# Performance work log

Hardware: AMD Instinct MI355X
Metric: run time of the kernel (lower is better)

The kernel has to match this reference:

```python
import jax, jax.numpy as jnp
import numpy as np

B, S, D, H = 4, 2048, 1024, 16
DH = D // H


def setup_inputs() -> dict:
    key = jax.random.key(0)
    ks = jax.random.split(key, 5)
    std = 1.0 / np.sqrt(D)
    return {
        "x": jax.random.normal(ks[0], (B, S, D), dtype=jnp.float32),
        "mask": jnp.ones((S, S), dtype=bool),  # unused by the original forward
        "Wq": jax.random.normal(ks[1], (D, D), dtype=jnp.float32) * std,
        "Wk": jax.random.normal(ks[2], (D, D), dtype=jnp.float32) * std,
        "Wv": jax.random.normal(ks[3], (D, D), dtype=jnp.float32) * std,
        "Wout": jax.random.normal(ks[4], (D, D), dtype=jnp.float32) * std,
    }


def reference(x, mask, Wq, Wk, Wv, Wout):
    n, s, d = x.shape
    scale = 1.0 / np.sqrt(DH).astype(np.float32)
    q = (x @ Wq).reshape(n, s, H, DH)
    k = (x @ Wk).reshape(n, s, H, DH)
    v = (x @ Wv).reshape(n, s, H, DH)
    # scores [n, q, k, h]; softmax over k axis (dim=-2 in original)
    attn = jnp.einsum('nqhd,nkhd->nqkh', q, k) * scale
    attn = jax.nn.softmax(attn, axis=-2)
    z = jnp.einsum('nqkh,nkhd->nqhd', attn, v).reshape(n, s, d)
    z = jnp.einsum('nqd,de->nqe', z, Wout)
    return x + z
```

## Files before the change

kernel.cpp:

```cpp
#include <hip/hip_runtime.h>

#define Bn 4
#define Sn 2048
#define Dn 1024
#define Hn 16
#define DHn 64

typedef float f32x4 __attribute__((ext_vector_type(4)));
typedef short bf16x8 __attribute__((ext_vector_type(8)));
typedef unsigned short u16;
typedef unsigned int u32;
typedef unsigned short u16x8 __attribute__((ext_vector_type(8)));
typedef unsigned short u16x4 __attribute__((ext_vector_type(4)));
typedef u32 u32x4 __attribute__((ext_vector_type(4)));

union B8 { u32x4 u; bf16x8 s; };

__device__ __forceinline__ u16 f2bf(float f){
  union { float f; u32 u; } v; v.f = f;
  return (u16)((v.u + 0x7fffu + ((v.u >> 16) & 1u)) >> 16);
}

__device__ __forceinline__ u32 pack_bf2(float lo, float hi){
  union { float f; u32 u; } a, b;
  a.f = lo; b.f = hi;
  return __builtin_amdgcn_perm(b.u + 0x8000u, a.u + 0x8000u, 0x07060302u);
}

#if __has_builtin(__builtin_amdgcn_exp2f)
#define EXP2(x) __builtin_amdgcn_exp2f(x)
#define QSCALE 0.18033688011112042f
#else
#define EXP2(x) __expf(x)
#define QSCALE 0.125f
#endif

#if __has_builtin(__builtin_amdgcn_global_load_lds)
#define G2L16(l, g) __builtin_amdgcn_global_load_lds((const __attribute__((address_space(1))) u32*)(g), \
                                                     (__attribute__((address_space(3))) u32*)(l), 16, 0, 0)
#else
#define G2L16(l, g) (*(bf16x8*)(l) = *(const bf16x8*)(g))
#endif

__global__ void cast_x_kernel(const float* __restrict__ x, u16* __restrict__ xb){
  size_t i = ((size_t)blockIdx.x * 256 + threadIdx.x) * 8;
  float4 f0 = *(const float4*)(x + i);
  float4 f1 = *(const float4*)(x + i + 4);
  u16x8 o;
  o[0]=f2bf(f0.x); o[1]=f2bf(f0.y); o[2]=f2bf(f0.z); o[3]=f2bf(f0.w);
  o[4]=f2bf(f1.x); o[5]=f2bf(f1.y); o[6]=f2bf(f1.z); o[7]=f2bf(f1.w);
  *(u16x8*)(xb + i) = o;
}

__global__ void cast_w_kernel(const float* __restrict__ w, u16* __restrict__ wt, float scale){
  __shared__ u16 tile[64*66];
  const int t = threadIdx.x;
  const int k0 = blockIdx.x * 64, n0 = blockIdx.y * 64;
  #pragma unroll
  for (int i = 0; i < 4; i++){
    int idx = i*256 + t;
    int r = idx >> 4, c4 = (idx & 15) * 4;
    float4 f = *(const float4*)(w + (size_t)(k0 + r)*Dn + n0 + c4);
    tile[r*66 + c4 + 0] = f2bf(f.x * scale);
    tile[r*66 + c4 + 1] = f2bf(f.y * scale);
    tile[r*66 + c4 + 2] = f2bf(f.z * scale);
    tile[r*66 + c4 + 3] = f2bf(f.w * scale);
  }
  __syncthreads();
  #pragma unroll
  for (int i = 0; i < 4; i++){
    int idx = i*256 + t;
    int nr = idx >> 4, kc4 = (idx & 15) * 4;
    u16x4 o;
    o[0] = tile[(kc4+0)*66 + nr];
    o[1] = tile[(kc4+1)*66 + nr];
    o[2] = tile[(kc4+2)*66 + nr];
    o[3] = tile[(kc4+3)*66 + nr];
    *(u16x4*)(wt + (size_t)(n0 + nr)*Dn + k0 + kc4) = o;
  }
}

__launch_bounds__(256)
__global__ void gemm_qkv_kernel(const u16* __restrict__ xb, const u16* __restrict__ wt_all,
                                u16* __restrict__ qb, u16* __restrict__ kb, u16* __restrict__ vb){
  __shared__ u16 As[128*32];
  __shared__ u16 Bs[128*32];
  const int t = threadIdx.x;
  const int wave = t >> 6, lane = t & 63;
  const int ln = lane & 15, quad = lane >> 4;
  const int wm = wave >> 1, wn = wave & 1;
  const int n0 = blockIdx.x * 128;
  const int m0 = blockIdx.y * 128;
  const int z  = blockIdx.z;
  const u16* wt = wt_all + (size_t)z * Dn * Dn;

  f32x4 acc[4][4] = {};

  for (int kt = 0; kt < Dn; kt += 32){
    __syncthreads();
    #pragma unroll
    for (int i = 0; i < 2; i++){
      int idx = i*256 + t;
      int r = idx >> 2, c8 = (idx & 3) * 8;
      G2L16(&As[idx*8], xb + (size_t)(m0 + r)*Dn + kt + c8);
      G2L16(&Bs[idx*8], wt + (size_t)(n0 + r)*Dn + kt + c8);
    }
    __syncthreads();
    bf16x8 a[4], b[4];
    #pragma unroll
    for (int rb = 0; rb < 4; rb++) a[rb] = *(const bf16x8*)&As[(wm*64 + rb*16 + ln)*32 + quad*8];
    #pragma unroll
    for (int cb = 0; cb < 4; cb++) b[cb] = *(const bf16x8*)&Bs[(wn*64 + cb*16 + ln)*32 + quad*8];
    #pragma unroll
    for (int rb = 0; rb < 4; rb++)
      #pragma unroll
      for (int cb = 0; cb < 4; cb++)
        acc[rb][cb] = __builtin_amdgcn_mfma_f32_16x16x32_bf16(a[rb], b[cb], acc[rb][cb], 0, 0, 0);
  }

  u16* outp = (z == 0) ? qb : (z == 1) ? kb : vb;
  #pragma unroll
  for (int rb = 0; rb < 4; rb++)
    #pragma unroll
    for (int cb = 0; cb < 4; cb++)
      #pragma unroll
      for (int reg = 0; reg < 4; reg++){
        int row = m0 + wm*64 + rb*16 + quad*4 + reg;
        int col = n0 + wn*64 + cb*16 + ln;
        int bb = row >> 11, s = row & 2047;
        int h = col >> 6, d = col & 63;
        outp[(((size_t)bb*Hn + h)*Sn + s)*DHn + d] = f2bf(acc[rb][cb][reg]);
      }
}

__global__ void transpose_v_kernel(const u16* __restrict__ v, u16* __restrict__ vt){
  __shared__ u16 tile[64*66];
  const int t = threadIdx.x;
  const int st = blockIdx.x;
  const int bh = blockIdx.y;
  const u16* src = v + ((size_t)bh * Sn + st*64) * DHn;
  u16* dst = vt + (size_t)bh * DHn * Sn + st*64;
  #pragma unroll
  for (int i = 0; i < 4; i++){
    int idx = i*256 + t;
    int r = idx >> 4, c4 = (idx & 15) * 4;
    u16x4 f = *(const u16x4*)(src + r*DHn + c4);
    tile[r*66 + c4+0] = f[0]; tile[r*66 + c4+1] = f[1];
    tile[r*66 + c4+2] = f[2]; tile[r*66 + c4+3] = f[3];
  }
  __syncthreads();
  #pragma unroll
  for (int i = 0; i < 4; i++){
    int idx = i*256 + t;
    int dr = idx >> 4, sc4 = (idx & 15) * 4;
    u16x4 o;
    o[0] = tile[(sc4+0)*66 + dr];
    o[1] = tile[(sc4+1)*66 + dr];
    o[2] = tile[(sc4+2)*66 + dr];
    o[3] = tile[(sc4+3)*66 + dr];
    *(u16x4*)(dst + (size_t)dr*Sn + sc4) = o;
  }
}

__launch_bounds__(256, 4)
__global__ void attn_kernel(const u16* q, const u16* __restrict__ k,
                            const u16* __restrict__ vt, u16* z){
  __shared__ u16 Ks[64*72];
  __shared__ u16 Vs[64*72];
  const int t = threadIdx.x;
  const int wave = t >> 6, lane = t & 63;
  const int ln = lane & 15, quad = lane >> 4;
  const int qt = blockIdx.x, h = blockIdx.y, b = blockIdx.z;
  const size_t bh = (size_t)b * Hn + h;
  const int q0 = qt*128 + wave*32;
  const u16* qp = q + bh * Sn * DHn;
  const u16* kp = k + bh * Sn * DHn;
  const u16* vp = vt + bh * DHn * Sn;

  bf16x8 qf[2][2];
  #pragma unroll
  for (int n = 0; n < 2; n++)
    #pragma unroll
    for (int kq = 0; kq < 2; kq++)
      qf[n][kq] = *(const bf16x8*)(qp + (size_t)(q0 + n*16 + ln)*DHn + kq*32 + quad*8);

  f32x4 zacc[4][2] = {};
  float dacc[2] = {0.f, 0.f};

  for (int kt = 0; kt < Sn/64; kt++){
    __syncthreads();
    #pragma unroll
    for (int i = 0; i < 2; i++){
      int idx = i*256 + t;
      int r = idx >> 3, c8 = (idx & 7) * 8;
      *(bf16x8*)&Ks[r*72 + c8] = *(const bf16x8*)(kp + (size_t)(kt*64 + r)*DHn + c8);
      *(bf16x8*)&Vs[r*72 + c8] = *(const bf16x8*)(vp + (size_t)r*Sn + kt*64 + c8);
    }
    __syncthreads();

    f32x4 sacc[4][2] = {};
    #pragma unroll
    for (int kq = 0; kq < 2; kq++){
      bf16x8 ka[4];
      #pragma unroll
      for (int mt = 0; mt < 4; mt++)
        ka[mt] = *(const bf16x8*)&Ks[(mt*16 + ln)*72 + kq*32 + quad*8];
      #pragma unroll
      for (int mt = 0; mt < 4; mt++)
        #pragma unroll
        for (int n = 0; n < 2; n++)
          sacc[mt][n] = __builtin_amdgcn_mfma_f32_16x16x32_bf16(ka[mt], qf[n][kq], sacc[mt][n], 0, 0, 0);
    }

    u32 pk[4][2][2];
    #pragma unroll
    for (int mt = 0; mt < 4; mt++)
      #pragma unroll
      for (int n = 0; n < 2; n++){
        f32x4 s = sacc[mt][n];
        float e0 = EXP2(s[0]), e1 = EXP2(s[1]), e2 = EXP2(s[2]), e3 = EXP2(s[3]);
        dacc[n] += (e0 + e1) + (e2 + e3);
        pk[mt][n][0] = pack_bf2(e0, e1);
        pk[mt][n][1] = pack_bf2(e2, e3);
      }

    #pragma unroll
    for (int ks = 0; ks < 2; ks++){
      B8 pb[2];
      #pragma unroll
      for (int n = 0; n < 2; n++)
        pb[n].u = (u32x4){pk[2*ks][n][0], pk[2*ks][n][1], pk[2*ks+1][n][0], pk[2*ks+1][n][1]};
      #pragma unroll
      for (int mtd = 0; mtd < 4; mtd++){
        const u16* vr = &Vs[(mtd*16 + ln)*72 + ks*32 + quad*4];
        uint2 v0 = *(const uint2*)vr;
        uint2 v1 = *(const uint2*)(vr + 16);
        B8 va; va.u = (u32x4){v0.x, v0.y, v1.x, v1.y};
        #pragma unroll
        for (int n = 0; n < 2; n++)
          zacc[mtd][n] = __builtin_amdgcn_mfma_f32_16x16x32_bf16(va.s, pb[n].s, zacc[mtd][n], 0, 0, 0);
      }
    }
  }

  float inv[2];
  #pragma unroll
  for (int n = 0; n < 2; n++){
    float d = dacc[n];
    d += __shfl_xor(d, 16, 64);
    d += __shfl_xor(d, 32, 64);
    inv[n] = 1.0f / d;
  }

  #pragma unroll
  for (int mtd = 0; mtd < 4; mtd++)
    #pragma unroll
    for (int n = 0; n < 2; n++){
      u16x4 o;
      #pragma unroll
      for (int j = 0; j < 4; j++) o[j] = f2bf(zacc[mtd][n][j] * inv[n]);
      *(u16x4*)(z + (bh*Sn + (size_t)(q0 + n*16 + ln))*DHn + mtd*16 + quad*4) = o;
    }
}

__launch_bounds__(256)
__global__ void gemm_out_kernel(const u16* __restrict__ zb, const u16* __restrict__ wt,
                                const float* __restrict__ x, float* __restrict__ out){
  __shared__ u16 As[128*32];
  __shared__ u16 Bs[128*32];
  const int t = threadIdx.x;
  const int wave = t >> 6, lane = t & 63;
  const int ln = lane & 15, quad = lane >> 4;
  const int wm = wave >> 1, wn = wave & 1;
  const int n0 = blockIdx.x * 128;
  const int m0 = blockIdx.y * 128;

  f32x4 acc[4][4] = {};

  for (int kt = 0; kt < Dn; kt += 32){
    int h = kt >> 6, d0 = kt & 63;
    __syncthreads();
    #pragma unroll
    for (int i = 0; i < 2; i++){
      int idx = i*256 + t;
      int r = idx >> 2, c8 = (idx & 3) * 8;
      int row = m0 + r;
      int bb = row >> 11, s = row & 2047;
      G2L16(&As[idx*8], zb + (((size_t)bb*Hn + h)*Sn + s)*DHn + d0 + c8);
      G2L16(&Bs[idx*8], wt + (size_t)(n0 + r)*Dn + kt + c8);
    }
    __syncthreads();
    bf16x8 a[4], b[4];
    #pragma unroll
    for (int rb = 0; rb < 4; rb++) a[rb] = *(const bf16x8*)&As[(wm*64 + rb*16 + ln)*32 + quad*8];
    #pragma unroll
    for (int cb = 0; cb < 4; cb++) b[cb] = *(const bf16x8*)&Bs[(wn*64 + cb*16 + ln)*32 + quad*8];
    #pragma unroll
    for (int rb = 0; rb < 4; rb++)
      #pragma unroll
      for (int cb = 0; cb < 4; cb++)
        acc[rb][cb] = __builtin_amdgcn_mfma_f32_16x16x32_bf16(a[rb], b[cb], acc[rb][cb], 0, 0, 0);
  }

  #pragma unroll
  for (int rb = 0; rb < 4; rb++)
    #pragma unroll
    for (int cb = 0; cb < 4; cb++)
      #pragma unroll
      for (int reg = 0; reg < 4; reg++){
        int row = m0 + wm*64 + rb*16 + quad*4 + reg;
        int col = n0 + wn*64 + cb*16 + ln;
        size_t off = (size_t)row*Dn + col;
        out[off] = acc[rb][cb][reg] + x[off];
      }
}

extern "C" void kernel_launch(void* const* d_in, const int* in_sizes, int n_in,
                              void* d_out, int out_size, void* d_ws, size_t ws_size,
                              hipStream_t stream){
  const float* x    = (const float*)d_in[0];
  const float* Wq   = (const float*)d_in[2];
  const float* Wk   = (const float*)d_in[3];
  const float* Wv   = (const float*)d_in[4];
  const float* Wout = (const float*)d_in[5];
  float* out = (float*)d_out;

  u16* ws = (u16*)d_ws;
  const size_t NW = (size_t)Dn * Dn;
  const size_t NX = (size_t)Bn * Sn * Dn;
  u16* wt  = ws;
  u16* xb  = wt + 4*NW;
  u16* qb  = xb + NX;
  u16* kb  = qb + NX;
  u16* vb  = kb + NX;
  u16* vtb = xb;

  dim3 blk(256);
  cast_x_kernel    <<<dim3((unsigned)(NX/(256*8))), blk, 0, stream>>>(x, xb);
  cast_w_kernel    <<<dim3(16,16), blk, 0, stream>>>(Wq,   wt,        QSCALE);
  cast_w_kernel    <<<dim3(16,16), blk, 0, stream>>>(Wk,   wt + NW,   1.0f);
  cast_w_kernel    <<<dim3(16,16), blk, 0, stream>>>(Wv,   wt + 2*NW, 1.0f);
  cast_w_kernel    <<<dim3(16,16), blk, 0, stream>>>(Wout, wt + 3*NW, 1.0f);
  gemm_qkv_kernel  <<<dim3(8,64,3), blk, 0, stream>>>(xb, wt, qb, kb, vb);
  transpose_v_kernel<<<dim3(32,64), blk, 0, stream>>>(vb, vtb);
  attn_kernel      <<<dim3(16,16,4), blk, 0, stream>>>(qb, kb, vtb, qb);
  gemm_out_kernel  <<<dim3(8,64), blk, 0, stream>>>(qb, wt + 3*NW, x, out);
}
```

Measured before the change: 310.9 us.

## Fuse V transpose into QKV GEMM epilogue, widen attention tiles, merge weight casts

Result: faster. 297.1 us (-4.4%).

```diff
diff --git a/kernel.cpp b/kernel.cpp
--- a/kernel.cpp
+++ b/kernel.cpp
@@ -52,10 +52,15 @@
   *(u16x8*)(xb + i) = o;
 }
 
-__global__ void cast_w_kernel(const float* __restrict__ w, u16* __restrict__ wt, float scale){
+__global__ void cast_w_kernel(const float* __restrict__ Wq, const float* __restrict__ Wk,
+                              const float* __restrict__ Wv, const float* __restrict__ Wo,
+                              u16* __restrict__ wt_all){
   __shared__ u16 tile[64*66];
   const int t = threadIdx.x;
-  const int k0 = blockIdx.x * 64, n0 = blockIdx.y * 64;
+  const int k0 = blockIdx.x * 64, n0 = blockIdx.y * 64, z = blockIdx.z;
+  const float* w = (z == 0) ? Wq : (z == 1) ? Wk : (z == 2) ? Wv : Wo;
+  const float scale = (z == 0) ? QSCALE : 1.0f;
+  u16* wt = wt_all + (size_t)z * Dn * Dn;
   #pragma unroll
   for (int i = 0; i < 4; i++){
     int idx = i*256 + t;
@@ -82,17 +87,18 @@
 
 __launch_bounds__(256)
 __global__ void gemm_qkv_kernel(const u16* __restrict__ xb, const u16* __restrict__ wt_all,
-                                u16* __restrict__ qb, u16* __restrict__ kb, u16* __restrict__ vb){
+                                u16* __restrict__ qb, u16* __restrict__ kb, u16* __restrict__ vtb){
   __shared__ u16 As[128*32];
   __shared__ u16 Bs[128*32];
+  __shared__ u16 Cs[128*136];
   const int t = threadIdx.x;
   const int wave = t >> 6, lane = t & 63;
   const int ln = lane & 15, quad = lane >> 4;
   const int wm = wave >> 1, wn = wave & 1;
   const int n0 = blockIdx.x * 128;
   const int m0 = blockIdx.y * 128;
-  const int z  = blockIdx.z;
-  const u16* wt = wt_all + (size_t)z * Dn * Dn;
+  const int zsel = blockIdx.z;
+  const u16* wt = wt_all + (size_t)zsel * Dn * Dn;
 
   f32x4 acc[4][4] = {};
 
@@ -118,51 +124,52 @@
         acc[rb][cb] = __builtin_amdgcn_mfma_f32_16x16x32_bf16(a[rb], b[cb], acc[rb][cb], 0, 0, 0);
   }
 
-  u16* outp = (z == 0) ? qb : (z == 1) ? kb : vb;
-  #pragma unroll
-  for (int rb = 0; rb < 4; rb++)
-    #pragma unroll
-    for (int cb = 0; cb < 4; cb++)
-      #pragma unroll
-      for (int reg = 0; reg < 4; reg++){
-        int row = m0 + wm*64 + rb*16 + quad*4 + reg;
-        int col = n0 + wn*64 + cb*16 + ln;
-        int bb = row >> 11, s = row & 2047;
-        int h = col >> 6, d = col & 63;
-        outp[(((size_t)bb*Hn + h)*Sn + s)*DHn + d] = f2bf(acc[rb][cb][reg]);
+  if (zsel < 2){
+    #pragma unroll
+    for (int rb = 0; rb < 4; rb++)
+      #pragma unroll
+      for (int cb = 0; cb < 4; cb++)
+        #pragma unroll
+        for (int reg = 0; reg < 4; reg++)
+          Cs[(wm*64 + rb*16 + quad*4 + reg)*136 + wn*64 + cb*16 + ln] = f2bf(acc[rb][cb][reg]);
+  } else {
+    #pragma unroll
+    for (int rb = 0; rb < 4; rb++)
+      #pragma unroll
+      for (int cb = 0; cb < 4; cb++){
+        u16x4 o;
+        #pragma unroll
+        for (int reg = 0; reg < 4; reg++) o[reg] = f2bf(acc[rb][cb][reg]);
+        *(u16x4*)&Cs[(wn*64 + cb*16 + ln)*136 + wm*64 + rb*16 + quad*4] = o;
       }
-}
-
-__global__ void transpose_v_kernel(const u16* __restrict__ v, u16* __restrict__ vt){
-  __shared__ u16 tile[64*66];
-  const int t = threadIdx.x;
-  const int st = blockIdx.x;
-  const int bh = blockIdx.y;
-  const u16* src = v + ((size_t)bh * Sn + st*64) * DHn;
-  u16* dst = vt + (size_t)bh * DHn * Sn + st*64;
-  #pragma unroll
-  for (int i = 0; i < 4; i++){
-    int idx = i*256 + t;
-    int r = idx >> 4, c4 = (idx & 15) * 4;
-    u16x4 f = *(const u16x4*)(src + r*DHn + c4);
-    tile[r*66 + c4+0] = f[0]; tile[r*66 + c4+1] = f[1];
-    tile[r*66 + c4+2] = f[2]; tile[r*66 + c4+3] = f[3];
   }
   __syncthreads();
-  #pragma unroll
-  for (int i = 0; i < 4; i++){
-    int idx = i*256 + t;
-    int dr = idx >> 4, sc4 = (idx & 15) * 4;
-    u16x4 o;
-    o[0] = tile[(sc4+0)*66 + dr];
-    o[1] = tile[(sc4+1)*66 + dr];
-    o[2] = tile[(sc4+2)*66 + dr];
-    o[3] = tile[(sc4+3)*66 + dr];
-    *(u16x4*)(dst + (size_t)dr*Sn + sc4) = o;
-  }
-}
-
-__launch_bounds__(256, 4)
+
+  if (zsel < 2){
+    u16* outp = (zsel == 0) ? qb : kb;
+    #pragma unroll
+    for (int i = 0; i < 8; i++){
+      int idx = i*256 + t;
+      int r = idx >> 4, c8 = (idx & 15) * 8;
+      bf16x8 vdat = *(const bf16x8*)&Cs[r*136 + c8];
+      int row = m0 + r, bb = row >> 11, s = row & 2047;
+      int col = n0 + c8, hh = col >> 6, d = col & 63;
+      *(bf16x8*)(outp + (((size_t)bb*Hn + hh)*Sn + s)*DHn + d) = vdat;
+    }
+  } else {
+    #pragma unroll
+    for (int i = 0; i < 8; i++){
+      int idx = i*256 + t;
+      int c = idx >> 4, r8 = (idx & 15) * 8;
+      bf16x8 vdat = *(const bf16x8*)&Cs[c*136 + r8];
+      int col = n0 + c, hh = col >> 6, d = col & 63;
+      int row = m0 + r8, bb = row >> 11, s = row & 2047;
+      *(bf16x8*)(vtb + (((size_t)bb*Hn + hh)*DHn + d)*Sn + s) = vdat;
+    }
+  }
+}
+
+__launch_bounds__(256, 2)
 __global__ void attn_kernel(const u16* q, const u16* __restrict__ k,
                             const u16* __restrict__ vt, u16* z){
   __shared__ u16 Ks[64*72];
@@ -172,20 +179,20 @@
   const int ln = lane & 15, quad = lane >> 4;
   const int qt = blockIdx.x, h = blockIdx.y, b = blockIdx.z;
   const size_t bh = (size_t)b * Hn + h;
-  const int q0 = qt*128 + wave*32;
+  const int q0 = qt*256 + wave*64;
   const u16* qp = q + bh * Sn * DHn;
   const u16* kp = k + bh * Sn * DHn;
   const u16* vp = vt + bh * DHn * Sn;
 
-  bf16x8 qf[2][2];
-  #pragma unroll
-  for (int n = 0; n < 2; n++)
+  bf16x8 qf[4][2];
+  #pragma unroll
+  for (int n = 0; n < 4; n++)
     #pragma unroll
     for (int kq = 0; kq < 2; kq++)
       qf[n][kq] = *(const bf16x8*)(qp + (size_t)(q0 + n*16 + ln)*DHn + kq*32 + quad*8);
 
-  f32x4 zacc[4][2] = {};
-  float dacc[2] = {0.f, 0.f};
+  f32x4 zacc[4][4] = {};
+  float dacc[4] = {0.f, 0.f, 0.f, 0.f};
 
   for (int kt = 0; kt < Sn/64; kt++){
     __syncthreads();
@@ -198,7 +205,7 @@
     }
     __syncthreads();
 
-    f32x4 sacc[4][2] = {};
+    f32x4 sacc[4][4] = {};
     #pragma unroll
     for (int kq = 0; kq < 2; kq++){
       bf16x8 ka[4];
@@ -208,15 +215,15 @@
       #pragma unroll
       for (int mt = 0; mt < 4; mt++)
         #pragma unroll
-        for (int n = 0; n < 2; n++)
+        for (int n = 0; n < 4; n++)
           sacc[mt][n] = __builtin_amdgcn_mfma_f32_16x16x32_bf16(ka[mt], qf[n][kq], sacc[mt][n], 0, 0, 0);
     }
 
-    u32 pk[4][2][2];
+    u32 pk[4][4][2];
     #pragma unroll
     for (int mt = 0; mt < 4; mt++)
       #pragma unroll
-      for (int n = 0; n < 2; n++){
+      for (int n = 0; n < 4; n++){
         f32x4 s = sacc[mt][n];
         float e0 = EXP2(s[0]), e1 = EXP2(s[1]), e2 = EXP2(s[2]), e3 = EXP2(s[3]);
         dacc[n] += (e0 + e1) + (e2 + e3);
@@ -226,9 +233,9 @@
 
     #pragma unroll
     for (int ks = 0; ks < 2; ks++){
-      B8 pb[2];
-      #pragma unroll
-      for (int n = 0; n < 2; n++)
+      B8 pb[4];
+      #pragma unroll
+      for (int n = 0; n < 4; n++)
         pb[n].u = (u32x4){pk[2*ks][n][0], pk[2*ks][n][1], pk[2*ks+1][n][0], pk[2*ks+1][n][1]};
       #pragma unroll
       for (int mtd = 0; mtd < 4; mtd++){
@@ -237,15 +244,15 @@
         uint2 v1 = *(const uint2*)(vr + 16);
         B8 va; va.u = (u32x4){v0.x, v0.y, v1.x, v1.y};
         #pragma unroll
-        for (int n = 0; n < 2; n++)
+        for (int n = 0; n < 4; n++)
           zacc[mtd][n] = __builtin_amdgcn_mfma_f32_16x16x32_bf16(va.s, pb[n].s, zacc[mtd][n], 0, 0, 0);
       }
     }
   }
 
-  float inv[2];
-  #pragma unroll
-  for (int n = 0; n < 2; n++){
+  float inv[4];
+  #pragma unroll
+  for (int n = 0; n < 4; n++){
     float d = dacc[n];
     d += __shfl_xor(d, 16, 64);
     d += __shfl_xor(d, 32, 64);
@@ -255,7 +262,7 @@
   #pragma unroll
   for (int mtd = 0; mtd < 4; mtd++)
     #pragma unroll
-    for (int n = 0; n < 2; n++){
+    for (int n = 0; n < 4; n++){
       u16x4 o;
       #pragma unroll
       for (int j = 0; j < 4; j++) o[j] = f2bf(zacc[mtd][n][j] * inv[n]);
@@ -332,17 +339,12 @@
   u16* xb  = wt + 4*NW;
   u16* qb  = xb + NX;
   u16* kb  = qb + NX;
-  u16* vb  = kb + NX;
-  u16* vtb = xb;
+  u16* vtb = kb + NX;
 
   dim3 blk(256);
-  cast_x_kernel    <<<dim3((unsigned)(NX/(256*8))), blk, 0, stream>>>(x, xb);
-  cast_w_kernel    <<<dim3(16,16), blk, 0, stream>>>(Wq,   wt,        QSCALE);
-  cast_w_kernel    <<<dim3(16,16), blk, 0, stream>>>(Wk,   wt + NW,   1.0f);
-  cast_w_kernel    <<<dim3(16,16), blk, 0, stream>>>(Wv,   wt + 2*NW, 1.0f);
-  cast_w_kernel    <<<dim3(16,16), blk, 0, stream>>>(Wout, wt + 3*NW, 1.0f);
-  gemm_qkv_kernel  <<<dim3(8,64,3), blk, 0, stream>>>(xb, wt, qb, kb, vb);
-  transpose_v_kernel<<<dim3(32,64), blk, 0, stream>>>(vb, vtb);
-  attn_kernel      <<<dim3(16,16,4), blk, 0, stream>>>(qb, kb, vtb, qb);
-  gemm_out_kernel  <<<dim3(8,64), blk, 0, stream>>>(qb, wt + 3*NW, x, out);
-}
+  cast_x_kernel   <<<dim3((unsigned)(NX/(256*8))), blk, 0, stream>>>(x, xb);
+  cast_w_kernel   <<<dim3(16,16,4), blk, 0, stream>>>(Wq, Wk, Wv, Wout, wt);
+  gemm_qkv_kernel <<<dim3(8,64,3), blk, 0, stream>>>(xb, wt, qb, kb, vtb);
+  attn_kernel     <<<dim3(8,16,4), blk, 0, stream>>>(qb, kb, vtb, qb);
+  gemm_out_kernel <<<dim3(8,64), blk, 0, stream>>>(qb, wt + 3*NW, x, out);
+}
```
